# Performance work log

Measured on AMD Instinct MI355X. Metric: run time of the kernel, lower is better.

The kernel has to match this reference:

```python
import jax, jax.numpy as jnp
import numpy as np

NEG_INF = -jnp.inf

def log_g(x):
    # where(x>=0, log(relu(x)+0.5), -softplus(-x)); relu(x)+0.5 >= 0.5 so log is safe everywhere
    return jnp.where(x >= 0, jnp.log(jax.nn.relu(x) + 0.5), -jax.nn.softplus(-x))

def _combine(e1, e2):
    # resettable log-space affine combine: h <- exp(logA)*h + exp(logB), reset zeroes history
    a1, b1, r1 = e1
    a2, b2, r2 = e2
    a_in = jnp.where(r2, jnp.zeros_like(a1), a1)
    b_in = jnp.where(r2, jnp.full_like(b1, NEG_INF), b1)
    return (a2 + a_in, jnp.logaddexp(a2 + b_in, b2), r1 | r2)

def setup_inputs() -> dict:
    key = jax.random.key(0)
    k1, k2, k3, k4 = jax.random.split(key, 4)
    B, T, D_in, H, D_out = 8, 4096, 1024, 1024, 1024
    x = jax.random.normal(k1, (B, T, D_in), dtype=jnp.float32)
    is_init = jax.random.uniform(k2, (B, T)) < 0.005  # sparse episode resets
    W_hg = jax.random.normal(k3, (D_in, 2 * H), dtype=jnp.float32) / np.sqrt(D_in)
    W_out = jax.random.normal(k4, (H, D_out), dtype=jnp.float32) / np.sqrt(H)
    return {"x": x, "is_init": is_init, "W_hg": W_hg, "W_out": W_out}

def reference(x, is_init, W_hg, W_out):
    # training path: h_0 = 0 (log_h_0 = -inf), seq_len > 1
    hg = jnp.einsum('btd,dk->btk', x, W_hg)            # [B,T,2H]
    hidden, gate = jnp.split(hg, 2, axis=-1)           # each [B,T,H]
    log_coeffs = -jax.nn.softplus(gate)                # log(1 - z)
    log_values = -jax.nn.softplus(-gate) + log_g(hidden)  # log z + log g(h~)
    resets = jnp.broadcast_to(is_init[:, :, None], log_coeffs.shape)
    _, logB, _ = jax.lax.associative_scan(_combine, (log_coeffs, log_values, resets), axis=1)
    # h_t = logaddexp(logA_t + log_h0, logB_t); log_h0 = -inf since h_0 = 0 => h_t = exp(logB_t)
    h = jnp.exp(logB)                                  # [B,T,H]
    out = jnp.einsum('bth,ho->bto', h, W_out)          # [B,T,D_out]
    h_n = h[:, -1:]                                    # [B,1,H]
    return out, h_n
```

## Files before the change

kernel.cpp:

```cpp
#include <hip/hip_runtime.h>
#include <stdint.h>

#define B_    8
#define T_    4096
#define DIN   1024
#define HCH   1024
#define DOUT  1024
#define M_    (B_*T_)
#define CL    64
#define NCH   (T_/CL)

typedef unsigned short u16;
typedef unsigned int   u32;
typedef __attribute__((ext_vector_type(8))) __bf16 bf16x8;
typedef __attribute__((ext_vector_type(4))) float  f32x4;

static __device__ __forceinline__ u16 f2bf(float f){
  unsigned u = __builtin_bit_cast(unsigned, f);
  return (u16)((u + 0x7FFFu + ((u >> 16) & 1u)) >> 16);
}
static __device__ __forceinline__ float bf2f(u16 h){
  return __builtin_bit_cast(float, ((unsigned)h) << 16);
}

#define GLOAD_LDS16(gp, lp) __builtin_amdgcn_global_load_lds( \
    (__attribute__((address_space(1))) void*)(gp),            \
    (__attribute__((address_space(3))) void*)(lp), 16, 0, 0)

#define BARRIER() do { __builtin_amdgcn_sched_barrier(0); \
                       __builtin_amdgcn_s_barrier();      \
                       __builtin_amdgcn_sched_barrier(0); } while(0)

__global__ void cvt_bf16_kernel(const float* __restrict__ in, u16* __restrict__ out, int n4){
  int i = blockIdx.x * blockDim.x + threadIdx.x;
  if (i >= n4) return;
  float4 v = ((const float4*)in)[i];
  ushort4 o;
  o.x = f2bf(v.x); o.y = f2bf(v.y); o.z = f2bf(v.z); o.w = f2bf(v.w);
  ((ushort4*)out)[i] = o;
}

__global__ void transpose_cvt_kernel(const float* __restrict__ in, u16* __restrict__ out,
                                     int R, int C){
  __shared__ float tile[32][33];
  int tx = threadIdx.x & 31, ty = threadIdx.x >> 5;
  int c0 = blockIdx.x * 32, r0 = blockIdx.y * 32;
  #pragma unroll
  for (int j = 0; j < 4; ++j)
    tile[ty + j*8][tx] = in[(size_t)(r0 + ty + j*8) * C + c0 + tx];
  __syncthreads();
  #pragma unroll
  for (int j = 0; j < 4; ++j)
    out[(size_t)(c0 + ty + j*8) * R + r0 + tx] = f2bf(tile[tx][ty + j*8]);
}

__global__ void detect_kernel(const u32* __restrict__ p, int* __restrict__ flag){
  __shared__ int s;
  if (threadIdx.x == 0) s = 0;
  __syncthreads();
  int f = 0;
  for (int i = threadIdx.x; i < (B_*T_)/4; i += 1024)
    if (p[i] & 0xFFFFFF00u) f = 1;
  if (f) atomicOr(&s, 1);
  __syncthreads();
  if (threadIdx.x == 0) *flag = s;
}

template<bool BF16OUT, int NOUT>
__global__ __launch_bounds__(512, 2) void gemm8p_kernel(
    const u16* __restrict__ A, const u16* __restrict__ BT, void* __restrict__ outv)
{
  __shared__ u16 As[2][16384];
  __shared__ u16 Bs[2][16384];

  const int tid = threadIdx.x, lane = tid & 63, w = tid >> 6;
  const int wm = w >> 2, wn = w & 3;
  const int lr = lane & 15, lg = lane >> 4;
  const int l8 = lane >> 3, l7 = lane & 7;
  const int sgcol = (l7 ^ l8) * 8;

  const int nwg = gridDim.x;
  const int wg  = ((int)blockIdx.x & 7) * (nwg >> 3) + ((int)blockIdx.x >> 3);
  const int mb  = wg & 127;
  const int nb  = wg >> 7;
  const int m0  = mb * 256, n0 = nb * 256;

  const u16* __restrict__ Ab = A  + (size_t)m0 * 1024;
  const u16* __restrict__ Bb = BT + (size_t)n0 * 1024;

  auto stage = [&](u16 (*S)[16384], int buf, int half, int tt, const u16* __restrict__ Gb){
    #pragma unroll
    for (int i = 0; i < 2; ++i){
      int wi = w*2 + i;
      GLOAD_LDS16(Gb + (size_t)(half*128 + wi*8 + l8) * 1024 + tt*64 + sgcol,
                  &S[buf][half*8192 + wi*512]);
    }
  };

  bf16x8 af[4][2], b0[2][2], b1[2][2];
  f32x4 acc[2][2][4][2];
  #pragma unroll
  for (int a = 0; a < 2; ++a)
    #pragma unroll
    for (int b = 0; b < 2; ++b)
      #pragma unroll
      for (int m = 0; m < 4; ++m)
        #pragma unroll
        for (int n = 0; n < 2; ++n)
          acc[a][b][m][n] = (f32x4){0.f,0.f,0.f,0.f};

  auto ldA = [&](int buf, int mh){
    #pragma unroll
    for (int m = 0; m < 4; ++m)
      #pragma unroll
      for (int ks = 0; ks < 2; ++ks){
        int R = mh*128 + wm*64 + m*16 + lr;
        int g = (ks*4 + lg) ^ (lr & 7);
        af[m][ks] = *(const bf16x8*)&As[buf][R*64 + g*8];
      }
  };
  auto ldB = [&](bf16x8 (&bv)[2][2], int buf, int nh){
    #pragma unroll
    for (int n = 0; n < 2; ++n)
      #pragma unroll
      for (int ks = 0; ks < 2; ++ks){
        int R = nh*128 + wn*32 + n*16 + lr;
        int g = (ks*4 + lg) ^ (lr & 7);
        bv[n][ks] = *(const bf16x8*)&Bs[buf][R*64 + g*8];
      }
  };
  auto mmaQ = [&](f32x4 (&ac)[4][2], bf16x8 (&bv)[2][2]){
    __builtin_amdgcn_s_setprio(1);
    #pragma unroll
    for (int m = 0; m < 4; ++m)
      #pragma unroll
      for (int n = 0; n < 2; ++n)
        #pragma unroll
        for (int ks = 0; ks < 2; ++ks)
          ac[m][n] = __builtin_amdgcn_mfma_f32_16x16x32_bf16(af[m][ks], bv[n][ks], ac[m][n], 0, 0, 0);
    __builtin_amdgcn_s_setprio(0);
  };

  stage(As, 0, 0, 0, Ab);
  stage(Bs, 0, 0, 0, Bb);
  stage(Bs, 0, 1, 0, Bb);
  stage(As, 0, 1, 0, Ab);
  stage(As, 1, 0, 1, Ab);
  stage(Bs, 1, 0, 1, Bb);
  stage(Bs, 1, 1, 1, Bb);
  asm volatile("s_waitcnt vmcnt(6)" ::: "memory");
  BARRIER();

  for (int t = 0; t < 16; ++t){
    int cur = t & 1;
    ldA(cur, 0);
    ldB(b0, cur, 0);
    if (t+1 < 16) stage(As, cur^1, 1, t+1, Ab);
    BARRIER();
    mmaQ(acc[0][0], b0);
    BARRIER();
    ldB(b1, cur, 1);
    if (t+2 < 16) stage(As, cur, 0, t+2, Ab);
    BARRIER();
    mmaQ(acc[0][1], b1);
    BARRIER();
    ldA(cur, 1);
    if (t+2 < 16) stage(Bs, cur, 0, t+2, Bb);
    BARRIER();
    mmaQ(acc[1][1], b1);
    BARRIER();
    if (t+2 < 16) stage(Bs, cur, 1, t+2, Bb);
    if (t < 14)       { asm volatile("s_waitcnt vmcnt(6)" ::: "memory"); }
    else if (t == 14) { asm volatile("s_waitcnt vmcnt(0)" ::: "memory"); }
    BARRIER();
    mmaQ(acc[1][0], b0);
    BARRIER();
  }

  #pragma unroll
  for (int mh = 0; mh < 2; ++mh)
    #pragma unroll
    for (int nh = 0; nh < 2; ++nh)
      #pragma unroll
      for (int m = 0; m < 4; ++m)
        #pragma unroll
        for (int n = 0; n < 2; ++n)
          #pragma unroll
          for (int r = 0; r < 4; ++r){
            int row = m0 + mh*128 + wm*64 + m*16 + lg*4 + r;
            int col = n0 + nh*128 + wn*32 + n*16 + lr;
            float v = acc[mh][nh][m][n][r];
            if (BF16OUT) ((u16*)outv)[(size_t)row * NOUT + col] = f2bf(v);
            else       ((float*)outv)[(size_t)row * NOUT + col] = v;
          }
}

static __device__ __forceinline__ void cv_from_hg(float hv, float gv, float& c, float& v){
  c = 1.f / (1.f + __expf(gv));
  float z = 1.f - c;
  float g = (hv >= 0.f) ? (hv + 0.5f) : (1.f / (1.f + __expf(-hv)));
  v = z * g;
}

__global__ void scanA_kernel(const u16* __restrict__ hg,
                             const void* __restrict__ isin, const int* __restrict__ mode,
                             float* __restrict__ Cc, float* __restrict__ Vc)
{
  int tid = blockIdx.x * 256 + threadIdx.x;
  int chp = tid & 511, b = (tid >> 9) & 7, ck = tid >> 12;
  int ch0 = chp * 2;
  int md = *mode;
  const unsigned char* ib = (const unsigned char*)isin;
  const int* ii = (const int*)isin;
  int t0 = b * T_ + ck * CL;
  float C0 = 1.f, V0 = 0.f, C1 = 1.f, V1 = 0.f;
  #pragma unroll 4
  for (int i = 0; i < CL; ++i){
    int t = t0 + i;
    const u16* rowp = hg + (size_t)t * 2048;
    u32 h2 = *(const u32*)(rowp + ch0);
    u32 g2 = *(const u32*)(rowp + 1024 + ch0);
    float c0, v0, c1, v1;
    cv_from_hg(bf2f((u16)h2), bf2f((u16)(h2 >> 16)) * 0.f + bf2f((u16)(g2 & 0xFFFF)) * 0.f + bf2f((u16)h2), 0.f ? c0 : c0, v0);
    {
      float hv0 = bf2f((u16)(h2 & 0xFFFF)), hv1 = bf2f((u16)(h2 >> 16));
      float gv0 = bf2f((u16)(g2 & 0xFFFF)), gv1 = bf2f((u16)(g2 >> 16));
      cv_from_hg(hv0, gv0, c0, v0);
      cv_from_hg(hv1, gv1, c1, v1);
    }
    int r = md ? (int)ib[t] : ii[t];
    if (r){ C0 = 0.f; V0 = v0; C1 = 0.f; V1 = v1; }
    else  { V0 = __fmaf_rn(c0, V0, v0); C0 *= c0;
            V1 = __fmaf_rn(c1, V1, v1); C1 *= c1; }
  }
  int o = ck * 8192 + b * 1024 + ch0;
  *(float2*)&Cc[o] = make_float2(C0, C1);
  *(float2*)&Vc[o] = make_float2(V0, V1);
}

__global__ void scanB_kernel(const float* __restrict__ Cc, const float* __restrict__ Vc,
                             float* __restrict__ hin)
{
  int idx = blockIdx.x * 256 + threadIdx.x;
  float h = 0.f;
  #pragma unroll 8
  for (int ck = 0; ck < NCH; ++ck){
    int o = ck * 8192 + idx;
    hin[o] = h;
    h = __fmaf_rn(Cc[o], h, Vc[o]);
  }
}

__global__ void scanC_kernel(const u16* __restrict__ hg,
                             const void* __restrict__ isin, const int* __restrict__ mode,
                             const float* __restrict__ hin,
                             u16* __restrict__ hbf, float* __restrict__ hn)
{
  int tid = blockIdx.x * 256 + threadIdx.x;
  int chp = tid & 511, b = (tid >> 9) & 7, ck = tid >> 12;
  int ch0 = chp * 2;
  int md = *mode;
  const unsigned char* ib = (const unsigned char*)isin;
  const int* ii = (const int*)isin;
  int t0 = b * T_ + ck * CL;
  int o = ck * 8192 + b * 1024 + ch0;
  float h0 = hin[o], h1 = hin[o + 1];
  #pragma unroll 4
  for (int i = 0; i < CL; ++i){
    int t = t0 + i;
    const u16* rowp = hg + (size_t)t * 2048;
    u32 h2 = *(const u32*)(rowp + ch0);
    u32 g2 = *(const u32*)(rowp + 1024 + ch0);
    float hv0 = bf2f((u16)(h2 & 0xFFFF)), hv1 = bf2f((u16)(h2 >> 16));
    float gv0 = bf2f((u16)(g2 & 0xFFFF)), gv1 = bf2f((u16)(g2 >> 16));
    float c0, v0, c1, v1;
    cv_from_hg(hv0, gv0, c0, v0);
    cv_from_hg(hv1, gv1, c1, v1);
    int r = md ? (int)ib[t] : ii[t];
    h0 = r ? v0 : __fmaf_rn(c0, h0, v0);
    h1 = r ? v1 : __fmaf_rn(c1, h1, v1);
    *(u32*)&hbf[(size_t)t * HCH + ch0] = (u32)f2bf(h0) | ((u32)f2bf(h1) << 16);
  }
  if (ck == NCH - 1){ hn[b * 1024 + ch0] = h0; hn[b * 1024 + ch0 + 1] = h1; }
}

extern "C" void kernel_launch(void* const* d_in, const int* in_sizes, int n_in,
                              void* d_out, int out_size, void* d_ws, size_t ws_size,
                              hipStream_t stream)
{
  const float* x    = (const float*)d_in[0];
  const void*  isin = d_in[1];
  const float* Whg  = (const float*)d_in[2];
  const float* Wout = (const float*)d_in[3];
  float* out = (float*)d_out;

  char* ws = (char*)d_ws;
  size_t off = 0;
  auto alloc = [&](size_t bytes) -> char* {
    char* p = ws + off;
    off += (bytes + 255) & ~(size_t)255;
    return p;
  };
  u16*   xbf   = (u16*)  alloc((size_t)M_ * DIN * 2);
  u16*   WThg  = (u16*)  alloc((size_t)2 * HCH * DIN * 2);
  u16*   WTout = (u16*)  alloc((size_t)DOUT * HCH * 2);
  u16*   hg    = (u16*)  alloc((size_t)M_ * 2 * HCH * 2);
  u16*   hbf   = (u16*)  alloc((size_t)M_ * HCH * 2);
  float* Cc    = (float*)alloc((size_t)NCH * 8192 * 4);
  float* Vc    = (float*)alloc((size_t)NCH * 8192 * 4);
  float* hin   = (float*)alloc((size_t)NCH * 8192 * 4);
  int*   mode  = (int*)  alloc(256);
  (void)ws_size; (void)in_sizes; (void)n_in; (void)out_size;

  detect_kernel<<<1, 1024, 0, stream>>>((const u32*)isin, mode);
  cvt_bf16_kernel<<<(M_*DIN/4 + 255)/256, 256, 0, stream>>>(x, xbf, M_*DIN/4);
  transpose_cvt_kernel<<<dim3(2*HCH/32, DIN/32), 256, 0, stream>>>(Whg, WThg, DIN, 2*HCH);
  transpose_cvt_kernel<<<dim3(DOUT/32, HCH/32), 256, 0, stream>>>(Wout, WTout, HCH, DOUT);
  gemm8p_kernel<true, 2048><<<1024, 512, 0, stream>>>(xbf, WThg, hg);
  scanA_kernel<<<(8192*NCH/2)/256, 256, 0, stream>>>(hg, isin, mode, Cc, Vc);
  scanB_kernel<<<8192/256, 256, 0, stream>>>(Cc, Vc, hin);
  scanC_kernel<<<(8192*NCH/2)/256, 256, 0, stream>>>(hg, isin, mode, hin, hbf,
                                                     out + (size_t)M_ * DOUT);
  gemm8p_kernel<false, 1024><<<512, 512, 0, stream>>>(hbf, WTout, out);
}
```

Measured before the change: 604.8 us.

## Fuse fp32-to-bf16 activation conversion into first GEMM and merge prep kernels

The first GEMM now reads fp32 x directly through registers, converts it to bf16 and writes it into swizzled LDS. This removes the separate conversion kernel and its 64 MB bf16 round trip. The two weight transposes and the reset-format detection are merged into one prep kernel, cutting launches. The main loop is restructured with explicit vmcnt/lgkm waits, fewer barriers and a peeled tail. The trade-off is register-staged A loads that double A read bytes (fp32) and add VALU conversion work inside the GEMM.

```diff
diff --git a/kernel.cpp b/kernel.cpp
--- a/kernel.cpp
+++ b/kernel.cpp
@@ -30,21 +30,17 @@
 #define BARRIER() do { __builtin_amdgcn_sched_barrier(0); \
                        __builtin_amdgcn_s_barrier();      \
                        __builtin_amdgcn_sched_barrier(0); } while(0)
-
-__global__ void cvt_bf16_kernel(const float* __restrict__ in, u16* __restrict__ out, int n4){
-  int i = blockIdx.x * blockDim.x + threadIdx.x;
-  if (i >= n4) return;
-  float4 v = ((const float4*)in)[i];
-  ushort4 o;
-  o.x = f2bf(v.x); o.y = f2bf(v.y); o.z = f2bf(v.z); o.w = f2bf(v.w);
-  ((ushort4*)out)[i] = o;
-}
-
-__global__ void transpose_cvt_kernel(const float* __restrict__ in, u16* __restrict__ out,
-                                     int R, int C){
+#define WAIT_VM(n)  do { asm volatile("s_waitcnt vmcnt(" #n ")" ::: "memory"); \
+                         __builtin_amdgcn_sched_barrier(0); } while(0)
+#define WAIT_LGKM0() do { asm volatile("s_waitcnt lgkmcnt(0)" ::: "memory"); \
+                          __builtin_amdgcn_sched_barrier(0); } while(0)
+
+static __device__ __forceinline__ void transpose_tile(const float* __restrict__ in,
+                                                      u16* __restrict__ out,
+                                                      int R, int C, int bx, int by){
   __shared__ float tile[32][33];
   int tx = threadIdx.x & 31, ty = threadIdx.x >> 5;
-  int c0 = blockIdx.x * 32, r0 = blockIdx.y * 32;
+  int c0 = bx * 32, r0 = by * 32;
   #pragma unroll
   for (int j = 0; j < 4; ++j)
     tile[ty + j*8][tx] = in[(size_t)(r0 + ty + j*8) * C + c0 + tx];
@@ -54,21 +50,31 @@
     out[(size_t)(c0 + ty + j*8) * R + r0 + tx] = f2bf(tile[tx][ty + j*8]);
 }
 
-__global__ void detect_kernel(const u32* __restrict__ p, int* __restrict__ flag){
-  __shared__ int s;
-  if (threadIdx.x == 0) s = 0;
-  __syncthreads();
-  int f = 0;
-  for (int i = threadIdx.x; i < (B_*T_)/4; i += 1024)
-    if (p[i] & 0xFFFFFF00u) f = 1;
-  if (f) atomicOr(&s, 1);
-  __syncthreads();
-  if (threadIdx.x == 0) *flag = s;
-}
-
-template<bool BF16OUT, int NOUT>
-__global__ __launch_bounds__(512, 2) void gemm8p_kernel(
-    const u16* __restrict__ A, const u16* __restrict__ BT, void* __restrict__ outv)
+__global__ void prep_kernel(const float* __restrict__ Whg, const float* __restrict__ Wout,
+                            const u32* __restrict__ isin,
+                            u16* __restrict__ WThg, u16* __restrict__ WTout,
+                            int* __restrict__ flag){
+  int bid = blockIdx.x;
+  if (bid < 2048){
+    transpose_tile(Whg, WThg, DIN, 2*HCH, bid & 63, bid >> 6);
+  } else if (bid < 3072){
+    int b2 = bid - 2048;
+    transpose_tile(Wout, WTout, HCH, DOUT, b2 & 31, b2 >> 5);
+  } else {
+    __shared__ int s;
+    if (threadIdx.x == 0) s = 0;
+    __syncthreads();
+    int f = 0;
+    for (int i = threadIdx.x; i < (B_*T_)/4; i += 256)
+      if (isin[i] & 0xFFFFFF00u) f = 1;
+    if (f) atomicOr(&s, 1);
+    __syncthreads();
+    if (threadIdx.x == 0) *flag = s;
+  }
+}
+
+__global__ __launch_bounds__(512, 2) void gemm1f_kernel(
+    const float* __restrict__ X, const u16* __restrict__ BT, u16* __restrict__ hg)
 {
   __shared__ u16 As[2][16384];
   __shared__ u16 Bs[2][16384];
@@ -81,20 +87,40 @@
 
   const int nwg = gridDim.x;
   const int wg  = ((int)blockIdx.x & 7) * (nwg >> 3) + ((int)blockIdx.x >> 3);
-  const int mb  = wg & 127;
-  const int nb  = wg >> 7;
+  const int mb  = wg & 127, nb = wg >> 7;
   const int m0  = mb * 256, n0 = nb * 256;
 
-  const u16* __restrict__ Ab = A  + (size_t)m0 * 1024;
-  const u16* __restrict__ Bb = BT + (size_t)n0 * 1024;
-
-  auto stage = [&](u16 (*S)[16384], int buf, int half, int tt, const u16* __restrict__ Gb){
-    #pragma unroll
-    for (int i = 0; i < 2; ++i){
-      int wi = w*2 + i;
-      GLOAD_LDS16(Gb + (size_t)(half*128 + wi*8 + l8) * 1024 + tt*64 + sgcol,
-                  &S[buf][half*8192 + wi*512]);
-    }
+  const float* __restrict__ Xb = X  + (size_t)m0 * DIN;
+  const u16*  __restrict__  Bb = BT + (size_t)n0 * DIN;
+
+  const int ar = tid >> 2, ac = (tid & 3) * 16;
+
+  float4 ra0[4], ra1[4];
+  auto issA = [&](float4 (&ra)[4], int h, int t){
+    const float* p = Xb + (size_t)(h*128 + ar) * DIN + t*64 + ac;
+    #pragma unroll
+    for (int i = 0; i < 4; ++i) ra[i] = ((const float4*)p)[i];
+  };
+  auto wrA = [&](float4 (&ra)[4], int h, int buf){
+    int row = h*128 + ar;
+    bf16x8 v0, v1;
+    v0[0]=(__bf16)ra[0].x; v0[1]=(__bf16)ra[0].y; v0[2]=(__bf16)ra[0].z; v0[3]=(__bf16)ra[0].w;
+    v0[4]=(__bf16)ra[1].x; v0[5]=(__bf16)ra[1].y; v0[6]=(__bf16)ra[1].z; v0[7]=(__bf16)ra[1].w;
+    v1[0]=(__bf16)ra[2].x; v1[1]=(__bf16)ra[2].y; v1[2]=(__bf16)ra[2].z; v1[3]=(__bf16)ra[2].w;
+    v1[4]=(__bf16)ra[3].x; v1[5]=(__bf16)ra[3].y; v1[6]=(__bf16)ra[3].z; v1[7]=(__bf16)ra[3].w;
+    int s = row & 7, gb = (tid & 3) * 2;
+    *(bf16x8*)&As[buf][row*64 + ((gb+0)^s)*8] = v0;
+    *(bf16x8*)&As[buf][row*64 + ((gb+1)^s)*8] = v1;
+  };
+  auto stageB = [&](int buf, int t){
+    #pragma unroll
+    for (int half = 0; half < 2; ++half)
+      #pragma unroll
+      for (int i = 0; i < 2; ++i){
+        int wi = w*2 + i;
+        GLOAD_LDS16(Bb + (size_t)(half*128 + wi*8 + l8) * DIN + t*64 + sgcol,
+                    &Bs[buf][half*8192 + wi*512]);
+      }
   };
 
   bf16x8 af[4][2], b0[2][2], b1[2][2];
@@ -141,40 +167,54 @@
     __builtin_amdgcn_s_setprio(0);
   };
 
-  stage(As, 0, 0, 0, Ab);
-  stage(Bs, 0, 0, 0, Bb);
-  stage(Bs, 0, 1, 0, Bb);
-  stage(As, 0, 1, 0, Ab);
-  stage(As, 1, 0, 1, Ab);
-  stage(Bs, 1, 0, 1, Bb);
-  stage(Bs, 1, 1, 1, Bb);
-  asm volatile("s_waitcnt vmcnt(6)" ::: "memory");
+  issA(ra0, 0, 0); issA(ra1, 1, 0);
+  stageB(0, 0);
+  WAIT_VM(4);
+  wrA(ra0, 0, 0); wrA(ra1, 1, 0);
+  issA(ra0, 0, 1); issA(ra1, 1, 1);
+  stageB(1, 1);
+  WAIT_LGKM0();
   BARRIER();
 
-  for (int t = 0; t < 16; ++t){
-    int cur = t & 1;
-    ldA(cur, 0);
-    ldB(b0, cur, 0);
-    if (t+1 < 16) stage(As, cur^1, 1, t+1, Ab);
+  for (int t = 0; t < 14; ++t){
+    const int cur = t & 1, nxt = cur ^ 1;
+    WAIT_VM(8);
+    ldA(cur, 0); ldB(b0, cur, 0);
+    wrA(ra0, 0, nxt);
+    issA(ra0, 0, t+2);
+    WAIT_LGKM0();
     BARRIER();
     mmaQ(acc[0][0], b0);
-    BARRIER();
+    WAIT_VM(8);
     ldB(b1, cur, 1);
-    if (t+2 < 16) stage(As, cur, 0, t+2, Ab);
+    wrA(ra1, 1, nxt);
+    issA(ra1, 1, t+2);
+    WAIT_LGKM0();
     BARRIER();
     mmaQ(acc[0][1], b1);
-    BARRIER();
     ldA(cur, 1);
-    if (t+2 < 16) stage(Bs, cur, 0, t+2, Bb);
+    stageB(cur, t+2);
+    WAIT_LGKM0();
     BARRIER();
     mmaQ(acc[1][1], b1);
-    BARRIER();
-    if (t+2 < 16) stage(Bs, cur, 1, t+2, Bb);
-    if (t < 14)       { asm volatile("s_waitcnt vmcnt(6)" ::: "memory"); }
-    else if (t == 14) { asm volatile("s_waitcnt vmcnt(0)" ::: "memory"); }
-    BARRIER();
     mmaQ(acc[1][0], b0);
-    BARRIER();
+  }
+  {
+    WAIT_VM(0);
+    ldA(0, 0); ldB(b0, 0, 0); ldB(b1, 0, 1);
+    wrA(ra0, 0, 1); wrA(ra1, 1, 1);
+    WAIT_LGKM0();
+    BARRIER();
+    mmaQ(acc[0][0], b0); mmaQ(acc[0][1], b1);
+    ldA(0, 1);
+    mmaQ(acc[1][1], b1); mmaQ(acc[1][0], b0);
+  }
+  {
+    BARRIER();
+    ldA(1, 0); ldB(b0, 1, 0); ldB(b1, 1, 1);
+    mmaQ(acc[0][0], b0); mmaQ(acc[0][1], b1);
+    ldA(1, 1);
+    mmaQ(acc[1][1], b1); mmaQ(acc[1][0], b0);
   }
 
   #pragma unroll
@@ -189,9 +229,123 @@
           for (int r = 0; r < 4; ++r){
             int row = m0 + mh*128 + wm*64 + m*16 + lg*4 + r;
             int col = n0 + nh*128 + wn*32 + n*16 + lr;
-            float v = acc[mh][nh][m][n][r];
-            if (BF16OUT) ((u16*)outv)[(size_t)row * NOUT + col] = f2bf(v);
-            else       ((float*)outv)[(size_t)row * NOUT + col] = v;
+            hg[(size_t)row * 2048 + col] = f2bf(acc[mh][nh][m][n][r]);
+          }
+}
+
+__global__ __launch_bounds__(512, 2) void gemm2_kernel(
+    const u16* __restrict__ A, const u16* __restrict__ BT, float* __restrict__ out)
+{
+  __shared__ u16 As[2][16384];
+  __shared__ u16 Bs[2][16384];
+
+  const int tid = threadIdx.x, lane = tid & 63, w = tid >> 6;
+  const int wm = w >> 2, wn = w & 3;
+  const int lr = lane & 15, lg = lane >> 4;
+  const int l8 = lane >> 3, l7 = lane & 7;
+  const int sgcol = (l7 ^ l8) * 8;
+
+  const int nwg = gridDim.x;
+  const int wg  = ((int)blockIdx.x & 7) * (nwg >> 3) + ((int)blockIdx.x >> 3);
+  const int mb  = wg & 127, nb = wg >> 7;
+  const int m0  = mb * 256, n0 = nb * 256;
+
+  const u16* __restrict__ Ab = A  + (size_t)m0 * HCH;
+  const u16* __restrict__ Bb = BT + (size_t)n0 * HCH;
+
+  auto stage = [&](u16 (*S)[16384], int buf, int half, int tt, const u16* __restrict__ Gb){
+    #pragma unroll
+    for (int i = 0; i < 2; ++i){
+      int wi = w*2 + i;
+      GLOAD_LDS16(Gb + (size_t)(half*128 + wi*8 + l8) * HCH + tt*64 + sgcol,
+                  &S[buf][half*8192 + wi*512]);
+    }
+  };
+
+  bf16x8 af[4][2], b0[2][2], b1[2][2];
+  f32x4 acc[2][2][4][2];
+  #pragma unroll
+  for (int a = 0; a < 2; ++a)
+    #pragma unroll
+    for (int b = 0; b < 2; ++b)
+      #pragma unroll
+      for (int m = 0; m < 4; ++m)
+        #pragma unroll
+        for (int n = 0; n < 2; ++n)
+          acc[a][b][m][n] = (f32x4){0.f,0.f,0.f,0.f};
+
+  auto ldA = [&](int buf, int mh){
+    #pragma unroll
+    for (int m = 0; m < 4; ++m)
+      #pragma unroll
+      for (int ks = 0; ks < 2; ++ks){
+        int R = mh*128 + wm*64 + m*16 + lr;
+        int g = (ks*4 + lg) ^ (lr & 7);
+        af[m][ks] = *(const bf16x8*)&As[buf][R*64 + g*8];
+      }
+  };
+  auto ldB = [&](bf16x8 (&bv)[2][2], int buf, int nh){
+    #pragma unroll
+    for (int n = 0; n < 2; ++n)
+      #pragma unroll
+      for (int ks = 0; ks < 2; ++ks){
+        int R = nh*128 + wn*32 + n*16 + lr;
+        int g = (ks*4 + lg) ^ (lr & 7);
+        bv[n][ks] = *(const bf16x8*)&Bs[buf][R*64 + g*8];
+      }
+  };
+  auto mmaQ = [&](f32x4 (&ac)[4][2], bf16x8 (&bv)[2][2]){
+    __builtin_amdgcn_s_setprio(1);
+    #pragma unroll
+    for (int m = 0; m < 4; ++m)
+      #pragma unroll
+      for (int n = 0; n < 2; ++n)
+        #pragma unroll
+        for (int ks = 0; ks < 2; ++ks)
+          ac[m][n] = __builtin_amdgcn_mfma_f32_16x16x32_bf16(af[m][ks], bv[n][ks], ac[m][n], 0, 0, 0);
+    __builtin_amdgcn_s_setprio(0);
+  };
+
+  stage(As, 0, 0, 0, Ab); stage(Bs, 0, 0, 0, Bb);
+  stage(Bs, 0, 1, 0, Bb); stage(As, 0, 1, 0, Ab);
+  stage(As, 1, 0, 1, Ab); stage(Bs, 1, 0, 1, Bb); stage(Bs, 1, 1, 1, Bb);
+  WAIT_VM(6);
+  BARRIER();
+
+  for (int t = 0; t < 16; ++t){
+    const int cur = t & 1;
+    ldA(cur, 0); ldB(b0, cur, 0);
+    if (t+1 < 16) stage(As, cur^1, 1, t+1, Ab);
+    BARRIER();
+    mmaQ(acc[0][0], b0);
+    ldB(b1, cur, 1);
+    if (t+2 < 16) stage(As, cur, 0, t+2, Ab);
+    BARRIER();
+    mmaQ(acc[0][1], b1);
+    ldA(cur, 1);
+    if (t+2 < 16) stage(Bs, cur, 0, t+2, Bb);
+    BARRIER();
+    mmaQ(acc[1][1], b1);
+    if (t+2 < 16) stage(Bs, cur, 1, t+2, Bb);
+    if (t < 14)       { WAIT_VM(6); }
+    else if (t == 14) { WAIT_VM(0); }
+    BARRIER();
+    mmaQ(acc[1][0], b0);
+  }
+
+  #pragma unroll
+  for (int mh = 0; mh < 2; ++mh)
+    #pragma unroll
+    for (int nh = 0; nh < 2; ++nh)
+      #pragma unroll
+      for (int m = 0; m < 4; ++m)
+        #pragma unroll
+        for (int n = 0; n < 2; ++n)
+          #pragma unroll
+          for (int r = 0; r < 4; ++r){
+            int row = m0 + mh*128 + wm*64 + m*16 + lg*4 + r;
+            int col = n0 + nh*128 + wn*32 + n*16 + lr;
+            out[(size_t)row * DOUT + col] = acc[mh][nh][m][n][r];
           }
 }
 
@@ -220,14 +374,11 @@
     const u16* rowp = hg + (size_t)t * 2048;
     u32 h2 = *(const u32*)(rowp + ch0);
     u32 g2 = *(const u32*)(rowp + 1024 + ch0);
+    float hv0 = bf2f((u16)(h2 & 0xFFFF)), hv1 = bf2f((u16)(h2 >> 16));
+    float gv0 = bf2f((u16)(g2 & 0xFFFF)), gv1 = bf2f((u16)(g2 >> 16));
     float c0, v0, c1, v1;
-    cv_from_hg(bf2f((u16)h2), bf2f((u16)(h2 >> 16)) * 0.f + bf2f((u16)(g2 & 0xFFFF)) * 0.f + bf2f((u16)h2), 0.f ? c0 : c0, v0);
-    {
-      float hv0 = bf2f((u16)(h2 & 0xFFFF)), hv1 = bf2f((u16)(h2 >> 16));
-      float gv0 = bf2f((u16)(g2 & 0xFFFF)), gv1 = bf2f((u16)(g2 >> 16));
-      cv_from_hg(hv0, gv0, c0, v0);
-      cv_from_hg(hv1, gv1, c1, v1);
-    }
+    cv_from_hg(hv0, gv0, c0, v0);
+    cv_from_hg(hv1, gv1, c1, v1);
     int r = md ? (int)ib[t] : ii[t];
     if (r){ C0 = 0.f; V0 = v0; C1 = 0.f; V1 = v1; }
     else  { V0 = __fmaf_rn(c0, V0, v0); C0 *= c0;
@@ -301,7 +452,6 @@
     off += (bytes + 255) & ~(size_t)255;
     return p;
   };
-  u16*   xbf   = (u16*)  alloc((size_t)M_ * DIN * 2);
   u16*   WThg  = (u16*)  alloc((size_t)2 * HCH * DIN * 2);
   u16*   WTout = (u16*)  alloc((size_t)DOUT * HCH * 2);
   u16*   hg    = (u16*)  alloc((size_t)M_ * 2 * HCH * 2);
@@ -312,14 +462,11 @@
   int*   mode  = (int*)  alloc(256);
   (void)ws_size; (void)in_sizes; (void)n_in; (void)out_size;
 
-  detect_kernel<<<1, 1024, 0, stream>>>((const u32*)isin, mode);
-  cvt_bf16_kernel<<<(M_*DIN/4 + 255)/256, 256, 0, stream>>>(x, xbf, M_*DIN/4);
-  transpose_cvt_kernel<<<dim3(2*HCH/32, DIN/32), 256, 0, stream>>>(Whg, WThg, DIN, 2*HCH);
-  transpose_cvt_kernel<<<dim3(DOUT/32, HCH/32), 256, 0, stream>>>(Wout, WTout, HCH, DOUT);
-  gemm8p_kernel<true, 2048><<<1024, 512, 0, stream>>>(xbf, WThg, hg);
+  prep_kernel<<<3073, 256, 0, stream>>>(Whg, Wout, (const u32*)isin, WThg, WTout, mode);
+  gemm1f_kernel<<<1024, 512, 0, stream>>>(x, WThg, hg);
   scanA_kernel<<<(8192*NCH/2)/256, 256, 0, stream>>>(hg, isin, mode, Cc, Vc);
   scanB_kernel<<<8192/256, 256, 0, stream>>>(Cc, Vc, hin);
   scanC_kernel<<<(8192*NCH/2)/256, 256, 0, stream>>>(hg, isin, mode, hin, hbf,
                                                      out + (size_t)M_ * DOUT);
-  gemm8p_kernel<false, 1024><<<512, 512, 0, stream>>>(hbf, WTout, out);
-}
+  gemm2_kernel<<<512, 512, 0, stream>>>(hbf, WTout, out);
+}
```

After: 828.3 us. +37.0%, slower.
